# Kernel optimization log

Measured on AMD Instinct MI355X. Metric: run time of the kernel, lower is better.

The kernel has to match this reference:

```python
import jax, jax.numpy as jnp
import numpy as np

NUM_CLASSES = 21
POS_T, NEG_T, ALPHA, GAMMA, EPS = 0.5, 0.4, 0.25, 2.0, 1e-6
NEG_FILL = -1e30  # sorts below any focal value (focal >= 0)


def _pairwise_iou(a, b):
    # a: [A,4], b: [T,4] -> [A,T]
    x1 = jnp.maximum(a[:, None, 0], b[None, :, 0])
    y1 = jnp.maximum(a[:, None, 1], b[None, :, 1])
    x2 = jnp.minimum(a[:, None, 2], b[None, :, 2])
    y2 = jnp.minimum(a[:, None, 3], b[None, :, 3])
    inter = jnp.clip(x2 - x1, 0) * jnp.clip(y2 - y1, 0)
    a1 = (a[:, 2] - a[:, 0]) * (a[:, 3] - a[:, 1])
    a2 = (b[:, 2] - b[:, 0]) * (b[:, 3] - b[:, 1])
    return inter / (a1[:, None] + a2[None, :] - inter + EPS)


def _giou_loss(b1, b2):
    # b1, b2: [N,4] -> [N]
    x1 = jnp.maximum(b1[:, 0], b2[:, 0]); y1 = jnp.maximum(b1[:, 1], b2[:, 1])
    x2 = jnp.minimum(b1[:, 2], b2[:, 2]); y2 = jnp.minimum(b1[:, 3], b2[:, 3])
    inter = jnp.clip(x2 - x1, 0) * jnp.clip(y2 - y1, 0)
    a1 = (b1[:, 2] - b1[:, 0]) * (b1[:, 3] - b1[:, 1])
    a2 = (b2[:, 2] - b2[:, 0]) * (b2[:, 3] - b2[:, 1])
    union = a1 + a2 - inter
    iou = inter / (union + EPS)
    ex1 = jnp.minimum(b1[:, 0], b2[:, 0]); ey1 = jnp.minimum(b1[:, 1], b2[:, 1])
    ex2 = jnp.maximum(b1[:, 2], b2[:, 2]); ey2 = jnp.maximum(b1[:, 3], b2[:, 3])
    enc = (ex2 - ex1) * (ey2 - ey1)
    giou = iou - (enc - union) / (enc + EPS)
    return 1.0 - giou


def _per_image(conf, bbox, tb, tl, anchors):
    # conf: [A,C], bbox: [A,4], tb: [T,4], tl: [T], anchors: [A,4]
    A, C = conf.shape
    ious = _pairwise_iou(anchors, tb)                 # [A,T]
    max_ious = ious.max(axis=1)
    best_t = jnp.argmax(ious, axis=1)                 # [A] best target per anchor
    pos = max_ious >= POS_T
    neg = max_ious < NEG_T
    best_a = jnp.argmax(ious, axis=0)                 # [T] force-match best anchor per GT
    pos = pos.at[best_a].set(True)
    neg = neg.at[best_a].set(False)

    conf_target = jax.nn.one_hot(tl[best_t], C, dtype=conf.dtype) * pos[:, None].astype(conf.dtype)
    probs = jax.nn.softmax(conf, axis=1)
    is_pos_cell = conf_target == 1.0
    pt = jnp.where(is_pos_cell, probs, 1.0 - probs)
    alpha_f = jnp.where(is_pos_cell, ALPHA, 1.0 - ALPHA)
    focal = -alpha_f * (1.0 - pt) ** GAMMA * jnp.log(jnp.clip(pt, EPS))  # [A,C]

    num_pos = pos.sum()
    n_neg = neg.sum()
    pos_sum = jnp.where(pos[:, None], focal, 0.0).sum()

    # hard-negative mining: descending sort of masked flattened focal, sum top-k
    neg_flat = jnp.where(neg[:, None], focal, NEG_FILL).reshape(-1)
    sorted_neg = jnp.sort(neg_flat)[::-1]
    idx = jnp.arange(neg_flat.shape[0])
    k = jnp.minimum(3 * num_pos, n_neg)
    topk_sum = jnp.where(idx < k, sorted_neg, 0.0).sum()
    denom = jnp.maximum(num_pos + k, 1).astype(conf.dtype)
    conf_pos = jnp.where(n_neg > 0, (pos_sum + topk_sum) / denom,
                         pos_sum / jnp.maximum(num_pos, 1).astype(conf.dtype))

    k2 = jnp.minimum(100, n_neg)
    top2_mean = jnp.where(idx < k2, sorted_neg, 0.0).sum() / jnp.maximum(k2, 1).astype(conf.dtype)
    conf_nopos = jnp.where(n_neg > 0, top2_mean, focal.mean())
    conf_loss = jnp.where(num_pos > 0, conf_pos, conf_nopos)

    matched = tb[best_t]                              # [A,4]
    giou_l = _giou_loss(bbox, matched)                # [A]
    d = bbox - matched
    ad = jnp.abs(d)
    l1 = jnp.where(ad < 1.0, 0.5 * d * d, ad - 0.5).mean(axis=1)
    per = giou_l + 0.5 * l1
    bbox_loss = jnp.where(num_pos > 0,
                          jnp.where(pos, per, 0.0).sum() / jnp.maximum(num_pos, 1).astype(conf.dtype),
                          0.0)
    return conf_loss, bbox_loss


def _loss(conf_pred, bbox_pred, anchors, target_boxes, target_labels):
    conf_l, bbox_l = jax.vmap(
        lambda c, b, tb, tl: _per_image(c, b, tb, tl, anchors)
    )(conf_pred, bbox_pred, target_boxes, target_labels)
    conf_loss = conf_l.mean()
    bbox_loss = bbox_l.mean()
    total = 1.0 * conf_loss + 1.0 * bbox_loss  # conf_weight = bbox_weight = 1.0
    return jnp.stack([total, conf_loss, bbox_loss])


def _rand_boxes(key, shape):
    k1, k2 = jax.random.split(key)
    xy1 = jax.random.uniform(k1, shape + (2,)) * 0.8
    wh = jax.random.uniform(k2, shape + (2,)) * 0.2 + 0.01
    return jnp.concatenate([xy1, xy1 + wh], axis=-1)


def setup_inputs() -> dict:
    key = jax.random.key(0)
    ks = jax.random.split(key, 5)
    B, A, T, C = 16, 65536, 32, NUM_CLASSES
    conf_pred = jax.random.normal(ks[0], (B, A, C), dtype=jnp.float32)
    bbox_pred = _rand_boxes(ks[1], (B, A))
    anchors = _rand_boxes(ks[2], (A,))
    target_boxes = _rand_boxes(ks[3], (B, T))
    target_labels = jax.random.randint(ks[4], (B, T), 1, C)
    return {"conf_pred": conf_pred, "bbox_pred": bbox_pred, "anchors": anchors,
            "target_boxes": target_boxes, "target_labels": target_labels}


def reference(conf_pred, bbox_pred, anchors, target_boxes, target_labels):
    return _loss(conf_pred, bbox_pred, anchors, target_boxes, target_labels)
```

## Files before the change

kernel.cpp:

```cpp
#include <hip/hip_runtime.h>


#define AN 65536
#define BN 16
#define TN 32
#define CN 21
#define NBA 2048
#define LCAPG (2 * 65536)
#define LCAP 10240
#define CHUNK 256
#define BUFC (CHUNK * CN)

struct BlockAcc { float pos_sum; float bbox_sum; unsigned np; unsigned nn; };
struct ImgParams { double pos; double bbox; unsigned np, nn, k, ve, act; };

__device__ __forceinline__ float box_area(float4 B) {
    return __fmul_rn(__fsub_rn(B.z, B.x), __fsub_rn(B.w, B.y));
}
__device__ __forceinline__ float iou_rcp(float4 A, float aa, float4 T, float ta) {
    float x1 = fmaxf(A.x, T.x), y1 = fmaxf(A.y, T.y);
    float x2 = fminf(A.z, T.z), y2 = fminf(A.w, T.w);
    float inter = __fmul_rn(fmaxf(__fsub_rn(x2, x1), 0.f), fmaxf(__fsub_rn(y2, y1), 0.f));
    float den = __fadd_rn(__fsub_rn(__fadd_rn(aa, ta), inter), 1e-6f);
    return __fmul_rn(inter, __builtin_amdgcn_rcpf(den));
}
__device__ __forceinline__ float row_prep(const float* __restrict__ row, float* __restrict__ c) {
#pragma unroll
    for (int j = 0; j < CN; ++j) c[j] = row[j];
    float m1[10];
#pragma unroll
    for (int j = 0; j < 10; ++j) m1[j] = fmaxf(c[j], c[j + 10]);
    float m2[5];
#pragma unroll
    for (int j = 0; j < 5; ++j) m2[j] = fmaxf(m1[j], m1[j + 5]);
    float ma = fmaxf(m2[0], m2[1]), mb = fmaxf(m2[2], m2[3]);
    float m = fmaxf(fmaxf(ma, mb), fmaxf(m2[4], c[20]));
#pragma unroll
    for (int j = 0; j < CN; ++j) c[j] = __expf(__fsub_rn(c[j], m));
    float s1[10];
#pragma unroll
    for (int j = 0; j < 10; ++j) s1[j] = __fadd_rn(c[j], c[j + 10]);
    float s2[5];
#pragma unroll
    for (int j = 0; j < 5; ++j) s2[j] = __fadd_rn(s1[j], s1[j + 5]);
    float sa = __fadd_rn(s2[0], s2[1]), sb = __fadd_rn(s2[2], s2[3]);
    float s = __fadd_rn(__fadd_rn(sa, sb), __fadd_rn(s2[4], c[20]));
    return __builtin_amdgcn_rcpf(s);
}
__device__ __forceinline__ float cell_focal(float cexp, float inv, bool cellpos) {
    float p = __fmul_rn(cexp, inv);
    float pt = cellpos ? p : __fsub_rn(1.0f, p);
    float af = cellpos ? 0.25f : 0.75f;
    float om = __fsub_rn(1.0f, pt);
    float lg = __logf(fmaxf(pt, 1e-6f));
    return __fmul_rn(__fmul_rn(__fmul_rn(-af, om), om), lg);
}
__device__ __forceinline__ unsigned focal_bits(float fo) {
    unsigned bits = __float_as_uint(fo);
    if (bits == 0x80000000u) bits = 0u;
    return bits;
}
__device__ __forceinline__ float bbox_per(float4 b1, float4 b2) {
    float x1 = fmaxf(b1.x, b2.x), y1 = fmaxf(b1.y, b2.y);
    float x2 = fminf(b1.z, b2.z), y2 = fminf(b1.w, b2.w);
    float inter = fmaxf(x2 - x1, 0.f) * fmaxf(y2 - y1, 0.f);
    float a1 = (b1.z - b1.x) * (b1.w - b1.y);
    float a2 = (b2.z - b2.x) * (b2.w - b2.y);
    float un = a1 + a2 - inter;
    float iou = inter / (un + 1e-6f);
    float ex1 = fminf(b1.x, b2.x), ey1 = fminf(b1.y, b2.y);
    float ex2 = fmaxf(b1.z, b2.z), ey2 = fmaxf(b1.w, b2.w);
    float enc = (ex2 - ex1) * (ey2 - ey1);
    float giou = iou - (enc - un) / (enc + 1e-6f);
    float gl = 1.0f - giou;
    float l1 = 0.f, d, ad;
    d = b1.x - b2.x; ad = fabsf(d); l1 += (ad < 1.f) ? (0.5f * d * d) : (ad - 0.5f);
    d = b1.y - b2.y; ad = fabsf(d); l1 += (ad < 1.f) ? (0.5f * d * d) : (ad - 0.5f);
    d = b1.z - b2.z; ad = fabsf(d); l1 += (ad < 1.f) ? (0.5f * d * d) : (ad - 0.5f);
    d = b1.w - b2.w; ad = fabsf(d); l1 += (ad < 1.f) ? (0.5f * d * d) : (ad - 0.5f);
    return gl + 0.5f * (l1 * 0.25f);
}
__device__ __forceinline__ unsigned mbcnt64(unsigned long long m) {
    return __builtin_amdgcn_mbcnt_hi((unsigned)(m >> 32),
           __builtin_amdgcn_mbcnt_lo((unsigned)m, 0u));
}

__global__ __launch_bounds__(256) void main_kernel(
    const float* __restrict__ conf, const float4* __restrict__ bboxp,
    const float4* __restrict__ anchors, const float4* __restrict__ tboxes,
    const int* __restrict__ tlabels,
    unsigned long long* __restrict__ gbest,
    unsigned* __restrict__ ahist, unsigned* __restrict__ maxb,
    BlockAcc* __restrict__ blockAcc)
{
    __shared__ float4 tbS[TN];
    __shared__ int tlS[TN];
    __shared__ float taS[TN];
    __shared__ float iouS[16][260];
    __shared__ unsigned ahp[NBA / 2];
    __shared__ float pbV[TN][16];
    __shared__ int   pbA[TN][16];
    __shared__ float rF[2][4];
    __shared__ unsigned rI[2][4];
    int b = blockIdx.y, tid = threadIdx.x;
    int a = blockIdx.x * 256 + tid;
    for (int i = tid; i < NBA / 2; i += 256) ahp[i] = 0u;
    if (tid < TN) {
        float4 T = tboxes[b * TN + tid];
        tbS[tid] = T; tlS[tid] = tlabels[b * TN + tid]; taS[tid] = box_area(T);
    }
    float4 ab = anchors[a];
    float aa = box_area(ab);
    __syncthreads();

    float best = -1.0f; int bt = 0;
#pragma unroll
    for (int h = 0; h < 2; ++h) {
#pragma unroll
        for (int t2 = 0; t2 < 16; ++t2) {
            int t = h * 16 + t2;
            float iou = iou_rcp(ab, aa, tbS[t], taS[t]);
            iouS[t2][tid] = iou;
            if (iou > best) { best = iou; bt = t; }
        }
        __syncthreads();
        {
            int t2 = tid & 15, pp = tid >> 4;
            const float4* rp = (const float4*)(&iouS[t2][pp * 16]);
            float bv = -1.f; int ba = 0;
#pragma unroll
            for (int q = 0; q < 4; ++q) {
                float4 v4 = rp[q];
                int i0 = pp * 16 + q * 4;
                if (v4.x > bv) { bv = v4.x; ba = i0 + 0; }
                if (v4.y > bv) { bv = v4.y; ba = i0 + 1; }
                if (v4.z > bv) { bv = v4.z; ba = i0 + 2; }
                if (v4.w > bv) { bv = v4.w; ba = i0 + 3; }
            }
            pbV[h * 16 + t2][pp] = bv; pbA[h * 16 + t2][pp] = ba;
        }
        __syncthreads();
    }
    if (tid < TN) {
        float bv = -1.f; int ba = 0;
#pragma unroll
        for (int pp = 0; pp < 16; ++pp) {
            float v = pbV[tid][pp];
            if (v > bv) { bv = v; ba = pbA[tid][pp]; }
        }
        unsigned ga = blockIdx.x * 256 + (unsigned)ba;
        unsigned long long key =
            (((unsigned long long)__float_as_uint(bv)) << 32) | (unsigned long long)(unsigned)(~ga);
        atomicMax(&gbest[b * TN + tid], key);
    }

    size_t idx = (size_t)b * AN + a;
    bool posA = best >= 0.5f;
    bool negA = best < 0.4f;
    float fs = 0.f, bper = 0.f;
    unsigned mbenc = 0u;
    if (posA || negA) {
        float c[CN];
        float inv = row_prep(conf + idx * CN, c);
        if (posA) {
            int label = tlS[bt];
#pragma unroll
            for (int j = 0; j < CN; ++j) fs += cell_focal(c[j], inv, j == label);
            bper = bbox_per(bboxp[idx], tbS[bt]);
        } else {
            float m1[10];
#pragma unroll
            for (int j = 0; j < 10; ++j) m1[j] = fmaxf(c[j], c[j + 10]);
            float m2[5];
#pragma unroll
            for (int j = 0; j < 5; ++j) m2[j] = fmaxf(m1[j], m1[j + 5]);
            float ma = fmaxf(m2[0], m2[1]), mb2 = fmaxf(m2[2], m2[3]);
            float cmax = fmaxf(fmaxf(ma, mb2), fmaxf(m2[4], c[20]));
            float fo = cell_focal(cmax, inv, false);
            unsigned mb = focal_bits(fo);
            mbenc = (mb << 1) | 1u;
            unsigned bin = mb >> 20;
            atomicAdd(&ahp[bin >> 1], 1u << ((bin & 1) << 4));
        }
    }
    maxb[idx] = mbenc;

    float vpos = posA ? fs : 0.f, vb = bper;
    unsigned inp = posA ? 1u : 0u, inn = negA ? 1u : 0u;
#pragma unroll
    for (int off = 32; off; off >>= 1) {
        vpos += __shfl_down(vpos, off, 64);
        vb   += __shfl_down(vb,   off, 64);
        inp  += __shfl_down(inp,  off, 64);
        inn  += __shfl_down(inn,  off, 64);
    }
    int wv = tid >> 6, ln = tid & 63;
    if (ln == 0) { rF[0][wv] = vpos; rF[1][wv] = vb; rI[0][wv] = inp; rI[1][wv] = inn; }
    __syncthreads();
    if (tid == 0) {
        BlockAcc ba2;
        ba2.pos_sum = rF[0][0] + rF[0][1] + rF[0][2] + rF[0][3];
        ba2.bbox_sum = rF[1][0] + rF[1][1] + rF[1][2] + rF[1][3];
        ba2.np = rI[0][0] + rI[0][1] + rI[0][2] + rI[0][3];
        ba2.nn = rI[1][0] + rI[1][1] + rI[1][2] + rI[1][3];
        blockAcc[b * 256 + blockIdx.x] = ba2;
    }
    for (int i = tid; i < NBA / 2; i += 256) {
        unsigned v = ahp[i];
        if (v) {
            if (v & 0xFFFFu) atomicAdd(&ahist[b * NBA + 2 * i], v & 0xFFFFu);
            if (v >> 16)     atomicAdd(&ahist[b * NBA + 2 * i + 1], v >> 16);
        }
    }
}

__global__ __launch_bounds__(1024) void tailA_kernel(
    const float* __restrict__ conf, const float4* __restrict__ bboxp,
    const float4* __restrict__ anchors, const float4* __restrict__ tboxes,
    const int* __restrict__ tlabels,
    const unsigned long long* __restrict__ gbest,
    const BlockAcc* __restrict__ blockAcc,
    const unsigned* __restrict__ ahist, unsigned* __restrict__ maxb,
    ImgParams* __restrict__ params)
{
    __shared__ unsigned hist[NBA];
    __shared__ unsigned scan_[1024];
    __shared__ unsigned gaS[TN];
    __shared__ float4 tbS[TN];
    __shared__ int tlS[TN];
    __shared__ float taS[TN];
    __shared__ float dps[TN], dbb[TN];
    __shared__ int dnp[TN], dnn[TN];
    __shared__ double sdbl[16];
    __shared__ unsigned suns[16];
    __shared__ double s_pos, s_bbox;
    __shared__ unsigned s_np, s_nn, s_k, s_act, s_ve;

    int b = blockIdx.x, tid = threadIdx.x;
    int wv = tid >> 6, ln = tid & 63;

    for (int i = tid; i < NBA; i += 1024) hist[i] = ahist[b * NBA + i];
    if (tid < TN) {
        gaS[tid] = ~(unsigned)(gbest[b * TN + tid] & 0xFFFFFFFFull);
        float4 T = tboxes[b * TN + tid];
        tbS[tid] = T; tlS[tid] = tlabels[b * TN + tid]; taS[tid] = box_area(T);
        dps[tid] = 0.f; dbb[tid] = 0.f; dnp[tid] = 0; dnn[tid] = 0;
    }
    __syncthreads();

    if (tid < TN) {
        bool doit = true;
        unsigned ga = gaS[tid];
        for (int u = 0; u < tid; ++u) if (gaS[u] == ga) doit = false;
        if (doit) {
            size_t idx = (size_t)b * AN + ga;
            float4 ab = anchors[ga];
            float aa = box_area(ab);
            float best = -1.f; int bt = 0;
#pragma unroll
            for (int t = 0; t < TN; ++t) {
                float iou = iou_rcp(ab, aa, tbS[t], taS[t]);
                if (iou > best) { best = iou; bt = t; }
            }
            if (best < 0.5f) {
                int label = tlS[bt];
                float c[CN];
                float inv = row_prep(conf + idx * CN, c);
                float fsv = 0.f;
#pragma unroll
                for (int j = 0; j < CN; ++j) fsv += cell_focal(c[j], inv, j == label);
                dps[tid] = fsv;
                dbb[tid] = bbox_per(bboxp[idx], tbS[bt]);
                dnp[tid] = 1;
                if (best < 0.4f) {
                    unsigned enc = maxb[idx];
                    atomicSub(&hist[enc >> 21], 1u);
                    maxb[idx] = 0u;
                    dnn[tid] = -1;
                }
            }
        }
    }
    __syncthreads();

    if (tid < 256) {
        BlockAcc ba = blockAcc[b * 256 + tid];
        double ps = (double)ba.pos_sum, bs = (double)ba.bbox_sum;
        unsigned np = ba.np, nn = ba.nn;
#pragma unroll
        for (int off = 32; off; off >>= 1) {
            ps += __shfl_down(ps, off, 64);
            bs += __shfl_down(bs, off, 64);
            np += __shfl_down(np, off, 64);
            nn += __shfl_down(nn, off, 64);
        }
        if (ln == 0) { sdbl[wv] = ps; sdbl[8 + wv] = bs; suns[wv] = np; suns[8 + wv] = nn; }
    }
    __syncthreads();
    if (tid == 0) {
        double dp = 0, db = 0; int cp = 0, cn = 0;
        for (int i = 0; i < TN; ++i) { dp += dps[i]; db += dbb[i]; cp += dnp[i]; cn += dnn[i]; }
        s_pos = sdbl[0] + sdbl[1] + sdbl[2] + sdbl[3] + dp;
        s_bbox = sdbl[8] + sdbl[9] + sdbl[10] + sdbl[11] + db;
        unsigned NP = (unsigned)((int)(suns[0] + suns[1] + suns[2] + suns[3]) + cp);
        unsigned NN = (unsigned)((int)(suns[8] + suns[9] + suns[10] + suns[11]) + cn);
        s_np = NP; s_nn = NN;
        unsigned k = min(3u * NP, NN);
        s_k = k;
        s_act = (NN > 0 && k > 0) ? 1u : 0u;
        s_ve = 0u;
    }
    __syncthreads();

    if (s_act) {
        unsigned k = s_k;
        unsigned lc0 = hist[tid * 2], lc1 = hist[tid * 2 + 1];
        unsigned cc = lc0 + lc1;
        scan_[tid] = cc;
        __syncthreads();
        for (int off = 1; off < 1024; off <<= 1) {
            unsigned v = (tid + off < 1024) ? scan_[tid + off] : 0u;
            __syncthreads();
            scan_[tid] += v;
            __syncthreads();
        }
        {
            unsigned above = (tid < 1023) ? scan_[tid + 1] : 0u;
            if (above < k && above + cc >= k) {
                unsigned bin = (above + lc1 >= k) ? (unsigned)(tid * 2 + 1) : (unsigned)(tid * 2);
                s_ve = (bin << 21) | 1u;
            }
        }
        __syncthreads();
    }
    if (tid == 0) {
        ImgParams P;
        P.pos = s_pos; P.bbox = s_bbox;
        P.np = s_np; P.nn = s_nn; P.k = s_k; P.ve = s_ve; P.act = s_act;
        params[b] = P;
    }
}

__global__ __launch_bounds__(256) void tailB_kernel(
    const float* __restrict__ conf, const unsigned* __restrict__ maxb,
    const ImgParams* __restrict__ params,
    float* __restrict__ list, unsigned* __restrict__ listCnt)
{
    __shared__ int candS[1024];
    __shared__ unsigned bufS[BUFC];
    __shared__ unsigned s_cnt, s_bcnt, s_gbase;
    int b = blockIdx.y, tid = threadIdx.x;
    unsigned act = params[b].act;
    if (!act) return;
    unsigned ve = params[b].ve;
    unsigned vbits = ve >> 1;
    int base = blockIdx.x * 1024;

    if (tid == 0) s_cnt = 0u;
    __syncthreads();

    const uint4* mb4 = (const uint4*)(maxb + (size_t)b * AN + base);
    uint4 m4 = mb4[tid];
    unsigned c0 = (m4.x >= ve), c1 = (m4.y >= ve), c2 = (m4.z >= ve), c3 = (m4.w >= ve);
    unsigned cnt = c0 + c1 + c2 + c3;
    unsigned pos = 0;
    if (cnt) pos = atomicAdd(&s_cnt, cnt);
    int a0 = base + tid * 4;
    if (c0) candS[pos++] = a0 + 0;
    if (c1) candS[pos++] = a0 + 1;
    if (c2) candS[pos++] = a0 + 2;
    if (c3) candS[pos++] = a0 + 3;
    __syncthreads();
    unsigned n = s_cnt;

    for (unsigned cbase = 0; cbase < n; cbase += CHUNK) {
        if (tid == 0) s_bcnt = 0u;
        __syncthreads();
        unsigned i = cbase + tid;
        if (i < n) {
            int a = candS[i];
            size_t idx = (size_t)b * AN + a;
            float c[CN];
            float inv = row_prep(conf + idx * CN, c);
#pragma unroll
            for (int j = 0; j < CN; ++j) {
                float fo = cell_focal(c[j], inv, false);
                unsigned bits = focal_bits(fo);
                bool hit = bits >= vbits;
                unsigned long long msk = __ballot(hit);
                if (hit) {
                    unsigned pre = mbcnt64(msk);
                    unsigned bb = 0;
                    if (pre == 0) bb = atomicAdd(&s_bcnt, (unsigned)__popcll(msk));
                    bb = __shfl(bb, (int)(__ffsll((long long)msk) - 1), 64);
                    bufS[bb + pre] = bits;
                }
            }
        }
        __syncthreads();
        unsigned ccnt = s_bcnt;
        if (ccnt) {
            if (tid == 0) s_gbase = atomicAdd(&listCnt[b * 16], ccnt);
            __syncthreads();
            unsigned gb = s_gbase;
            for (unsigned j2 = tid; j2 < ccnt; j2 += 256) {
                unsigned p = gb + j2;
                if (p < (unsigned)LCAPG)
                    list[(size_t)b * LCAPG + p] = __uint_as_float(bufS[j2]);
            }
        }
        __syncthreads();
    }
}

__global__ __launch_bounds__(1024) void tailC_kernel(
    const float* __restrict__ list, const unsigned* __restrict__ listCnt,
    const ImgParams* __restrict__ params,
    double* __restrict__ imgRes, unsigned* __restrict__ ctr,
    float* __restrict__ out)
{
    __shared__ float lcache[LCAP];
    __shared__ unsigned hist[4096];
    __shared__ unsigned scan_[1024];
    __shared__ double sdbl[16];
    __shared__ double s_sumAbove;
    __shared__ unsigned s_b1, s_rem, s_b2, s_rem2, s_b3, s_rem3;

    int b = blockIdx.x, tid = threadIdx.x;
    int wv = tid >> 6, ln = tid & 63;
    ImgParams P = params[b];
    double topk = 0.0;

    if (P.act) {
        unsigned n = min(listCnt[b * 16], (unsigned)LCAPG);
        const float* gl = list + (size_t)b * LCAPG;
        bool inL = (n <= (unsigned)LCAP);
        if (inL) for (unsigned i = tid; i < n; i += 1024) lcache[i] = gl[i];
        if (tid == 0) { s_b1 = 0; s_rem = 0; s_b3 = 0; s_rem3 = 0; }
        for (int i = tid; i < 4096; i += 1024) hist[i] = 0u;
        __syncthreads();

        for (unsigned i = tid; i < n; i += 1024) {
            unsigned bits = __float_as_uint(inL ? lcache[i] : gl[i]);
            atomicAdd(&hist[bits >> 20], 1u);
        }
        __syncthreads();

        unsigned lc0 = hist[tid * 2], lc1 = hist[tid * 2 + 1];
        unsigned cc = lc0 + lc1;
        scan_[tid] = cc;
        __syncthreads();
        for (int off = 1; off < 1024; off <<= 1) {
            unsigned v = (tid + off < 1024) ? scan_[tid + off] : 0u;
            __syncthreads();
            scan_[tid] += v;
            __syncthreads();
        }
        {
            unsigned total = scan_[0];
            unsigned above = (tid < 1023) ? scan_[tid + 1] : 0u;
            unsigned r = min(P.k, total);
            if (r > 0 && above < r && above + cc >= r) {
                if (above + lc1 >= r) { s_b1 = (unsigned)(tid * 2 + 1); s_rem = r - above; }
                else { s_b1 = (unsigned)(tid * 2); s_rem = r - above - lc1; }
            }
        }
        __syncthreads();
        unsigned b1 = s_b1, rem = s_rem;

        for (int i = tid; i < 4096; i += 1024) hist[i] = 0u;
        __syncthreads();
        double sA = 0.0;
        for (unsigned i = tid; i < n; i += 1024) {
            float v = inL ? lcache[i] : gl[i];
            unsigned bits = __float_as_uint(v);
            unsigned hi = bits >> 20;
            if (hi > b1) sA += (double)v;
            else if (hi == b1) atomicAdd(&hist[(bits >> 8) & 0xFFFu], 1u);
        }
#pragma unroll
        for (int off = 32; off; off >>= 1) sA += __shfl_down(sA, off, 64);
        if (ln == 0) sdbl[wv] = sA;
        __syncthreads();
        if (tid == 0) {
            double tt = 0;
            for (int w = 0; w < 16; ++w) tt += sdbl[w];
            s_sumAbove = tt;
        }
        __syncthreads();
        double sumAbove = s_sumAbove;

        if (rem == 0) {
            topk = sumAbove;
        } else {
            unsigned l4[4], cc4 = 0;
#pragma unroll
            for (int q = 0; q < 4; ++q) { l4[q] = hist[tid * 4 + q]; cc4 += l4[q]; }
            scan_[tid] = cc4;
            __syncthreads();
            for (int off = 1; off < 1024; off <<= 1) {
                unsigned v = (tid + off < 1024) ? scan_[tid + off] : 0u;
                __syncthreads();
                scan_[tid] += v;
                __syncthreads();
            }
            {
                unsigned total = scan_[0];
                unsigned above = (tid < 1023) ? scan_[tid + 1] : 0u;
                unsigned r = min(rem, total);
                if (above < r && above + cc4 >= r) {
                    unsigned a2 = above;
                    for (int i = 3; i >= 0; --i) {
                        unsigned bc = l4[i];
                        if (a2 + bc >= r) { s_b2 = (unsigned)(tid * 4 + i); s_rem2 = r - a2; break; }
                        a2 += bc;
                    }
                }
            }
            __syncthreads();
            unsigned b2 = s_b2, rem2 = s_rem2;
            if (tid < 256) hist[tid] = 0u;
            __syncthreads();

            double sMid = 0.0;
            for (unsigned i = tid; i < n; i += 1024) {
                float v = inL ? lcache[i] : gl[i];
                unsigned bits = __float_as_uint(v);
                if ((bits >> 20) != b1) continue;
                unsigned sub = (bits >> 8) & 0xFFFu;
                if (sub > b2) sMid += (double)v;
                else if (sub == b2) atomicAdd(&hist[bits & 0xFFu], 1u);
            }
            __syncthreads();
            if (tid < 256) scan_[tid] = hist[tid];
            __syncthreads();
            for (int off = 1; off < 256; off <<= 1) {
                unsigned v = 0;
                if (tid < 256 && tid + off < 256) v = scan_[tid + off];
                __syncthreads();
                if (tid < 256) scan_[tid] += v;
                __syncthreads();
            }
            if (tid < 256) {
                unsigned above8 = (tid < 255) ? scan_[tid + 1] : 0u;
                unsigned c8 = hist[tid];
                if (above8 < rem2 && above8 + c8 >= rem2) { s_b3 = (unsigned)tid; s_rem3 = rem2 - above8; }
            }
            __syncthreads();
            unsigned b3 = s_b3, rem3 = s_rem3;

            double s3 = 0.0;
            for (unsigned i = tid; i < n; i += 1024) {
                float v = inL ? lcache[i] : gl[i];
                unsigned bits = __float_as_uint(v);
                if ((bits >> 20) == b1 && ((bits >> 8) & 0xFFFu) == b2 && (bits & 0xFFu) > b3)
                    s3 += (double)v;
            }
            double tot = sMid + s3;
#pragma unroll
            for (int off = 32; off; off >>= 1) tot += __shfl_down(tot, off, 64);
            if (ln == 0) sdbl[wv] = tot;
            __syncthreads();
            if (tid == 0) {
                double totAll = 0;
                for (int w = 0; w < 16; ++w) totAll += sdbl[w];
                unsigned vb3 = (b1 << 20) | (b2 << 8) | b3;
                topk = sumAbove + totAll + (double)rem3 * (double)__uint_as_float(vb3);
            }
        }
    }

    if (tid == 0) {
        double confl;
        if (P.act) confl = (P.pos + topk) / (double)max(P.np + P.k, 1u);
        else       confl = P.pos / (double)max(P.np, 1u);
        imgRes[b * 2 + 0] = confl;
        imgRes[b * 2 + 1] = P.bbox / (double)max(P.np, 1u);
        __threadfence();
        unsigned prev = atomicAdd(ctr, 1u);
        if (prev == BN - 1) {
            __threadfence();
            double cs = 0, bs = 0;
            for (int i = 0; i < BN; ++i) { cs += imgRes[i * 2]; bs += imgRes[i * 2 + 1]; }
            cs /= BN; bs /= BN;
            out[0] = (float)(cs + bs);
            out[1] = (float)cs;
            out[2] = (float)bs;
        }
    }
}

extern "C" void kernel_launch(void* const* d_in, const int* in_sizes, int n_in,
                              void* d_out, int out_size, void* d_ws, size_t ws_size,
                              hipStream_t stream)
{
    (void)in_sizes; (void)n_in; (void)out_size; (void)ws_size;
    const float*  conf    = (const float*)d_in[0];
    const float4* bboxp   = (const float4*)d_in[1];
    const float4* anchors = (const float4*)d_in[2];
    const float4* tboxes  = (const float4*)d_in[3];
    const int*    tlabels = (const int*)d_in[4];
    float* out = (float*)d_out;
    char* ws = (char*)d_ws;
    size_t off = 0;
    auto alloc = [&](size_t bytes) -> void* {
        void* p = (void*)(ws + off);
        off = (off + bytes + 255) & ~(size_t)255;
        return p;
    };
    unsigned*  maxb     = (unsigned*)alloc((size_t)BN * AN * 4);
    float*     list     = (float*)alloc((size_t)BN * LCAPG * 4);
    BlockAcc*  blockAcc = (BlockAcc*)alloc((size_t)BN * 256 * sizeof(BlockAcc));
    double*    imgRes   = (double*)alloc((size_t)BN * 2 * 8);
    ImgParams* params   = (ImgParams*)alloc((size_t)BN * sizeof(ImgParams));
    size_t zstart = off;
    unsigned long long* gbest = (unsigned long long*)alloc((size_t)BN * TN * 8);
    unsigned* ahist   = (unsigned*)alloc((size_t)BN * NBA * 4);
    unsigned* ctr     = (unsigned*)alloc(256);
    unsigned* listCnt = (unsigned*)alloc((size_t)BN * 16 * 4);
    size_t zbytes = off - zstart;
    hipMemsetAsync(ws + zstart, 0, zbytes, stream);

    dim3 gridA(AN / 256, BN);
    main_kernel<<<gridA, 256, 0, stream>>>(conf, bboxp, anchors, tboxes, tlabels,
                                           gbest, ahist, maxb, blockAcc);
    tailA_kernel<<<BN, 1024, 0, stream>>>(conf, bboxp, anchors, tboxes, tlabels,
                                          gbest, blockAcc, ahist, maxb, params);
    tailB_kernel<<<dim3(64, BN), 256, 0, stream>>>(conf, maxb, params, list, listCnt);
    tailC_kernel<<<BN, 1024, 0, stream>>>(list, listCnt, params, imgRes, ctr, out);
}
```

Before: 202.6 us.

## Fuse per-image tail reduction into main kernel via last-block counter

Removes the separate tailA kernel launch by having the last block per image (detected with an atomic counter and threadfence) perform the forced-match fixup, block-sum reduction and histogram threshold scan. The scan is reworked for 256 threads with 8 bins per thread, and shared iou buffer is reused for the histogram. It also replaces the per-negative-anchor max computation with exp(0)=1 since the softmax max element always has exp value 1. This saves a launch and a dependency gap, at the cost of a serialized tail inside the last block and extra shared memory.

```diff
diff --git a/kernel.cpp b/kernel.cpp
--- a/kernel.cpp
+++ b/kernel.cpp
@@ -24,9 +24,7 @@
     float den = __fadd_rn(__fsub_rn(__fadd_rn(aa, ta), inter), 1e-6f);
     return __fmul_rn(inter, __builtin_amdgcn_rcpf(den));
 }
-__device__ __forceinline__ float row_prep(const float* __restrict__ row, float* __restrict__ c) {
-#pragma unroll
-    for (int j = 0; j < CN; ++j) c[j] = row[j];
+__device__ __forceinline__ float row_prep_vals(float* __restrict__ c) {
     float m1[10];
 #pragma unroll
     for (int j = 0; j < 10; ++j) m1[j] = fmaxf(c[j], c[j + 10]);
@@ -46,6 +44,11 @@
     float sa = __fadd_rn(s2[0], s2[1]), sb = __fadd_rn(s2[2], s2[3]);
     float s = __fadd_rn(__fadd_rn(sa, sb), __fadd_rn(s2[4], c[20]));
     return __builtin_amdgcn_rcpf(s);
+}
+__device__ __forceinline__ float row_prep(const float* __restrict__ row, float* __restrict__ c) {
+#pragma unroll
+    for (int j = 0; j < CN; ++j) c[j] = row[j];
+    return row_prep_vals(c);
 }
 __device__ __forceinline__ float cell_focal(float cexp, float inv, bool cellpos) {
     float p = __fmul_rn(cexp, inv);
@@ -91,7 +94,8 @@
     const int* __restrict__ tlabels,
     unsigned long long* __restrict__ gbest,
     unsigned* __restrict__ ahist, unsigned* __restrict__ maxb,
-    BlockAcc* __restrict__ blockAcc)
+    BlockAcc* __restrict__ blockAcc,
+    ImgParams* __restrict__ params, unsigned* __restrict__ ctrA)
 {
     __shared__ float4 tbS[TN];
     __shared__ int tlS[TN];
@@ -102,6 +106,11 @@
     __shared__ int   pbA[TN][16];
     __shared__ float rF[2][4];
     __shared__ unsigned rI[2][4];
+    __shared__ double sdblA[8];
+    __shared__ unsigned sunsA[8];
+    __shared__ double s_pos, s_bbox;
+    __shared__ unsigned s_np, s_nn, s_k, s_act, s_ve, sFlagS;
+
     int b = blockIdx.y, tid = threadIdx.x;
     int a = blockIdx.x * 256 + tid;
     for (int i = tid; i < NBA / 2; i += 256) ahp[i] = 0u;
@@ -168,15 +177,7 @@
             for (int j = 0; j < CN; ++j) fs += cell_focal(c[j], inv, j == label);
             bper = bbox_per(bboxp[idx], tbS[bt]);
         } else {
-            float m1[10];
-#pragma unroll
-            for (int j = 0; j < 10; ++j) m1[j] = fmaxf(c[j], c[j + 10]);
-            float m2[5];
-#pragma unroll
-            for (int j = 0; j < 5; ++j) m2[j] = fmaxf(m1[j], m1[j + 5]);
-            float ma = fmaxf(m2[0], m2[1]), mb2 = fmaxf(m2[2], m2[3]);
-            float cmax = fmaxf(fmaxf(ma, mb2), fmaxf(m2[4], c[20]));
-            float fo = cell_focal(cmax, inv, false);
+            float fo = cell_focal(1.0f, inv, false);
             unsigned mb = focal_bits(fo);
             mbenc = (mb << 1) | 1u;
             unsigned bin = mb >> 20;
@@ -212,81 +213,71 @@
             if (v >> 16)     atomicAdd(&ahist[b * NBA + 2 * i + 1], v >> 16);
         }
     }
-}
-
-__global__ __launch_bounds__(1024) void tailA_kernel(
-    const float* __restrict__ conf, const float4* __restrict__ bboxp,
-    const float4* __restrict__ anchors, const float4* __restrict__ tboxes,
-    const int* __restrict__ tlabels,
-    const unsigned long long* __restrict__ gbest,
-    const BlockAcc* __restrict__ blockAcc,
-    const unsigned* __restrict__ ahist, unsigned* __restrict__ maxb,
-    ImgParams* __restrict__ params)
-{
-    __shared__ unsigned hist[NBA];
-    __shared__ unsigned scan_[1024];
-    __shared__ unsigned gaS[TN];
-    __shared__ float4 tbS[TN];
-    __shared__ int tlS[TN];
-    __shared__ float taS[TN];
-    __shared__ float dps[TN], dbb[TN];
-    __shared__ int dnp[TN], dnn[TN];
-    __shared__ double sdbl[16];
-    __shared__ unsigned suns[16];
-    __shared__ double s_pos, s_bbox;
-    __shared__ unsigned s_np, s_nn, s_k, s_act, s_ve;
-
-    int b = blockIdx.x, tid = threadIdx.x;
-    int wv = tid >> 6, ln = tid & 63;
-
-    for (int i = tid; i < NBA; i += 1024) hist[i] = ahist[b * NBA + i];
+    __syncthreads();
+
+    if (tid == 0) {
+        __threadfence();
+        unsigned prev = atomicAdd(&ctrA[b * 16], 1u);
+        sFlagS = (prev == (unsigned)(AN / 256) - 1u) ? 1u : 0u;
+    }
+    __syncthreads();
+    if (!sFlagS) return;
+    __threadfence();
+
+    unsigned* histL = (unsigned*)&iouS[0][0];
+    unsigned* scanL = histL + 2048;
+    float*    dpsL  = (float*)(scanL + 256);
+    float*    dbbL  = dpsL + TN;
+    int*      dnpL  = (int*)(dbbL + TN);
+    int*      dnnL  = dnpL + TN;
+    unsigned* gaL   = (unsigned*)(dnnL + TN);
+
+    for (int i = tid; i < NBA; i += 256) histL[i] = ahist[b * NBA + i];
     if (tid < TN) {
-        gaS[tid] = ~(unsigned)(gbest[b * TN + tid] & 0xFFFFFFFFull);
-        float4 T = tboxes[b * TN + tid];
-        tbS[tid] = T; tlS[tid] = tlabels[b * TN + tid]; taS[tid] = box_area(T);
-        dps[tid] = 0.f; dbb[tid] = 0.f; dnp[tid] = 0; dnn[tid] = 0;
+        gaL[tid] = ~(unsigned)(gbest[b * TN + tid] & 0xFFFFFFFFull);
+        dpsL[tid] = 0.f; dbbL[tid] = 0.f; dnpL[tid] = 0; dnnL[tid] = 0;
     }
     __syncthreads();
 
     if (tid < TN) {
         bool doit = true;
-        unsigned ga = gaS[tid];
-        for (int u = 0; u < tid; ++u) if (gaS[u] == ga) doit = false;
+        unsigned ga = gaL[tid];
+        for (int u = 0; u < tid; ++u) if (gaL[u] == ga) doit = false;
         if (doit) {
-            size_t idx = (size_t)b * AN + ga;
-            float4 ab = anchors[ga];
-            float aa = box_area(ab);
-            float best = -1.f; int bt = 0;
+            size_t idx2 = (size_t)b * AN + ga;
+            float4 ab2 = anchors[ga];
+            float aa2 = box_area(ab2);
+            float best2 = -1.f; int bt2 = 0;
 #pragma unroll
             for (int t = 0; t < TN; ++t) {
-                float iou = iou_rcp(ab, aa, tbS[t], taS[t]);
-                if (iou > best) { best = iou; bt = t; }
-            }
-            if (best < 0.5f) {
-                int label = tlS[bt];
-                float c[CN];
-                float inv = row_prep(conf + idx * CN, c);
+                float iou = iou_rcp(ab2, aa2, tbS[t], taS[t]);
+                if (iou > best2) { best2 = iou; bt2 = t; }
+            }
+            if (best2 < 0.5f) {
+                int label = tlS[bt2];
+                float c2[CN];
+                float inv2 = row_prep(conf + idx2 * CN, c2);
                 float fsv = 0.f;
 #pragma unroll
-                for (int j = 0; j < CN; ++j) fsv += cell_focal(c[j], inv, j == label);
-                dps[tid] = fsv;
-                dbb[tid] = bbox_per(bboxp[idx], tbS[bt]);
-                dnp[tid] = 1;
-                if (best < 0.4f) {
-                    unsigned enc = maxb[idx];
-                    atomicSub(&hist[enc >> 21], 1u);
-                    maxb[idx] = 0u;
-                    dnn[tid] = -1;
+                for (int j = 0; j < CN; ++j) fsv += cell_focal(c2[j], inv2, j == label);
+                dpsL[tid] = fsv;
+                dbbL[tid] = bbox_per(bboxp[idx2], tbS[bt2]);
+                dnpL[tid] = 1;
+                if (best2 < 0.4f) {
+                    unsigned enc = maxb[idx2];
+                    atomicSub(&histL[enc >> 21], 1u);
+                    maxb[idx2] = 0u;
+                    dnnL[tid] = -1;
                 }
             }
         }
     }
     __syncthreads();
 
-    if (tid < 256) {
-        BlockAcc ba = blockAcc[b * 256 + tid];
-        double ps = (double)ba.pos_sum, bs = (double)ba.bbox_sum;
-        unsigned np = ba.np, nn = ba.nn;
+    {
+        BlockAcc ba3 = blockAcc[b * 256 + tid];
+        double ps = (double)ba3.pos_sum, bs = (double)ba3.bbox_sum;
+        unsigned np = ba3.np, nn = ba3.nn;
 #pragma unroll
         for (int off = 32; off; off >>= 1) {
             ps += __shfl_down(ps, off, 64);
@@ -294,16 +285,16 @@
             np += __shfl_down(np, off, 64);
             nn += __shfl_down(nn, off, 64);
         }
-        if (ln == 0) { sdbl[wv] = ps; sdbl[8 + wv] = bs; suns[wv] = np; suns[8 + wv] = nn; }
+        if (ln == 0) { sdblA[wv] = ps; sdblA[4 + wv] = bs; sunsA[wv] = np; sunsA[4 + wv] = nn; }
     }
     __syncthreads();
     if (tid == 0) {
         double dp = 0, db = 0; int cp = 0, cn = 0;
-        for (int i = 0; i < TN; ++i) { dp += dps[i]; db += dbb[i]; cp += dnp[i]; cn += dnn[i]; }
-        s_pos = sdbl[0] + sdbl[1] + sdbl[2] + sdbl[3] + dp;
-        s_bbox = sdbl[8] + sdbl[9] + sdbl[10] + sdbl[11] + db;
-        unsigned NP = (unsigned)((int)(suns[0] + suns[1] + suns[2] + suns[3]) + cp);
-        unsigned NN = (unsigned)((int)(suns[8] + suns[9] + suns[10] + suns[11]) + cn);
+        for (int i = 0; i < TN; ++i) { dp += dpsL[i]; db += dbbL[i]; cp += dnpL[i]; cn += dnnL[i]; }
+        s_pos = sdblA[0] + sdblA[1] + sdblA[2] + sdblA[3] + dp;
+        s_bbox = sdblA[4] + sdblA[5] + sdblA[6] + sdblA[7] + db;
+        unsigned NP = (unsigned)((int)(sunsA[0] + sunsA[1] + sunsA[2] + sunsA[3]) + cp);
+        unsigned NN = (unsigned)((int)(sunsA[4] + sunsA[5] + sunsA[6] + sunsA[7]) + cn);
         s_np = NP; s_nn = NN;
         unsigned k = min(3u * NP, NN);
         s_k = k;
@@ -314,21 +305,26 @@
 
     if (s_act) {
         unsigned k = s_k;
-        unsigned lc0 = hist[tid * 2], lc1 = hist[tid * 2 + 1];
-        unsigned cc = lc0 + lc1;
-        scan_[tid] = cc;
-        __syncthreads();
-        for (int off = 1; off < 1024; off <<= 1) {
-            unsigned v = (tid + off < 1024) ? scan_[tid + off] : 0u;
-            __syncthreads();
-            scan_[tid] += v;
+        unsigned l8[8], cc = 0;
+#pragma unroll
+        for (int q = 0; q < 8; ++q) { l8[q] = histL[tid * 8 + q]; cc += l8[q]; }
+        scanL[tid] = cc;
+        __syncthreads();
+        for (int off = 1; off < 256; off <<= 1) {
+            unsigned v = (tid + off < 256) ? scanL[tid + off] : 0u;
+            __syncthreads();
+            scanL[tid] += v;
             __syncthreads();
         }
         {
-            unsigned above = (tid < 1023) ? scan_[tid + 1] : 0u;
+            unsigned above = (tid < 255) ? scanL[tid + 1] : 0u;
             if (above < k && above + cc >= k) {
-                unsigned bin = (above + lc1 >= k) ? (unsigned)(tid * 2 + 1) : (unsigned)(tid * 2);
-                s_ve = (bin << 21) | 1u;
+                unsigned a2 = above;
+                for (int q = 7; q >= 0; --q) {
+                    unsigned bc = l8[q];
+                    if (a2 + bc >= k) { s_ve = ((unsigned)(tid * 8 + q) << 21) | 1u; break; }
+                    a2 += bc;
+                }
             }
         }
         __syncthreads();
@@ -618,14 +614,13 @@
     unsigned* ahist   = (unsigned*)alloc((size_t)BN * NBA * 4);
     unsigned* ctr     = (unsigned*)alloc(256);
     unsigned* listCnt = (unsigned*)alloc((size_t)BN * 16 * 4);
+    unsigned* ctrA    = (unsigned*)alloc((size_t)BN * 16 * 4);
     size_t zbytes = off - zstart;
     hipMemsetAsync(ws + zstart, 0, zbytes, stream);
 
     dim3 gridA(AN / 256, BN);
     main_kernel<<<gridA, 256, 0, stream>>>(conf, bboxp, anchors, tboxes, tlabels,
-                                           gbest, ahist, maxb, blockAcc);
-    tailA_kernel<<<BN, 1024, 0, stream>>>(conf, bboxp, anchors, tboxes, tlabels,
-                                          gbest, blockAcc, ahist, maxb, params);
+                                           gbest, ahist, maxb, blockAcc, params, ctrA);
     tailB_kernel<<<dim3(64, BN), 256, 0, stream>>>(conf, maxb, params, list, listCnt);
     tailC_kernel<<<BN, 1024, 0, stream>>>(list, listCnt, params, imgRes, ctr, out);
 }
```

After: 353.7 us. 74.6% more time.
